# Optimization experiments

Measured on AMD Instinct MI355X. Metric: run time of the kernel, lower is better.

The kernel has to match this reference:

```python
import jax, jax.numpy as jnp
import numpy as np

B, S, H = 1, 2048, 4096
NQ, NKV = 32, 8
HD = H // NQ  # 128


def _rope_tables(seq_len, head_dim, base=10000.0):
    inv_freq = 1.0 / (base ** (np.arange(0, head_dim, 2, dtype=np.float32) / head_dim))
    t = np.arange(seq_len, dtype=np.float32)
    freqs = np.outer(t, inv_freq)  # (S, HD/2)
    emb = np.concatenate([freqs, freqs], axis=-1)  # (S, HD)
    return jnp.asarray(np.cos(emb)), jnp.asarray(np.sin(emb))


def setup_inputs() -> dict:
    key = jax.random.key(0)
    ks = jax.random.split(key, 5)
    cos, sin = _rope_tables(S, HD)
    scale = 1.0 / np.sqrt(H)
    return {
        "hidden_states": jax.random.normal(ks[0], (B, S, H), dtype=jnp.float32),
        "cos": cos,
        "sin": sin,
        "wq": jax.random.normal(ks[1], (H, NQ * HD), dtype=jnp.float32) * scale,
        "wk": jax.random.normal(ks[2], (H, NKV * HD), dtype=jnp.float32) * scale,
        "wv": jax.random.normal(ks[3], (H, NKV * HD), dtype=jnp.float32) * scale,
        "wo": jax.random.normal(ks[4], (NQ * HD, H), dtype=jnp.float32) * scale,
    }


def _rotate_half(x):
    x1, x2 = jnp.split(x, 2, axis=-1)
    return jnp.concatenate([-x2, x1], axis=-1)


def reference(hidden_states, cos, sin, wq, wk, wv, wo):
    b, s, _ = hidden_states.shape
    q = (hidden_states @ wq).reshape(b, s, NQ, HD)
    k = (hidden_states @ wk).reshape(b, s, NKV, HD)
    v = (hidden_states @ wv).reshape(b, s, NKV, HD)
    c = cos[None, :, None, :]
    sn = sin[None, :, None, :]
    q = q * c + _rotate_half(q) * sn
    k = k * c + _rotate_half(k) * sn
    groups = NQ // NKV
    # GQA: compute scores per kv-head group without materially repeating K/V beyond einsum
    q = q.reshape(b, s, NKV, groups, HD)
    # scores: (b, kv_head, group, s_q, s_k)
    scores = jnp.einsum("bqhgd,bkhd->bhgqk", q, k) / jnp.sqrt(jnp.asarray(HD, q.dtype))
    causal = jnp.tril(jnp.ones((s, s), dtype=bool))
    scores = jnp.where(causal[None, None, None], scores, jnp.finfo(scores.dtype).min)
    attn = jax.nn.softmax(scores, axis=-1)
    out = jnp.einsum("bhgqk,bkhd->bqhgd", attn, v)  # (b, s, kv_h, g, d)
    out = out.reshape(b, s, NQ * HD)
    return out @ wo
```

## Files before the change

kernel.cpp:

```cpp
#include <hip/hip_runtime.h>
#include <hip/hip_bf16.h>
#include <math.h>

#define S_LEN 2048
#define HDIM  4096
#define NQ_H  32
#define NKV_H 8
#define HD_   128
#define DQ (NQ_H*HD_)
#define DKV (NKV_H*HD_)
#define NFUSE (DQ + 2*DKV)

typedef unsigned short u16;
typedef unsigned int   u32;
typedef __attribute__((ext_vector_type(8))) short short8;
typedef __attribute__((ext_vector_type(4))) float f32x4;

__device__ __forceinline__ u16 bf16_rne(float x) {
    u32 u = __float_as_uint(x);
    u = (u + 0x7FFFu + ((u >> 16) & 1u)) >> 16;
    return (u16)u;
}
__device__ __forceinline__ float bf16_to_f(u16 h) {
    return __uint_as_float(((u32)h) << 16);
}
__device__ __forceinline__ void glds16(const u16* g, u16* l) {
    __builtin_amdgcn_global_load_lds(
        (const __attribute__((address_space(1))) u32*)g,
        (__attribute__((address_space(3))) u32*)l,
        16, 0, 0);
}

__global__ __launch_bounds__(256) void cvt_bf16(const float* __restrict__ in,
                                                u16* __restrict__ out, int n) {
    int i = (blockIdx.x * 256 + threadIdx.x) * 8;
    if (i >= n) return;
    float4 a = *(const float4*)&in[i];
    float4 b = *(const float4*)&in[i + 4];
    u16 h[8];
    h[0] = bf16_rne(a.x); h[1] = bf16_rne(a.y); h[2] = bf16_rne(a.z); h[3] = bf16_rne(a.w);
    h[4] = bf16_rne(b.x); h[5] = bf16_rne(b.y); h[6] = bf16_rne(b.z); h[7] = bf16_rne(b.w);
    *(uint4*)&out[i] = *(uint4*)h;
}

__global__ __launch_bounds__(256) void add_f32(const float* __restrict__ p1,
                                               float* __restrict__ out, int n) {
    int i = (blockIdx.x * 256 + threadIdx.x) * 4;
    if (i >= n) return;
    float4 a = *(const float4*)&out[i];
    float4 b = *(const float4*)&p1[i];
    a.x += b.x; a.y += b.y; a.z += b.z; a.w += b.w;
    *(float4*)&out[i] = a;
}

__global__ __launch_bounds__(256) void cvtT_qkv(const float* __restrict__ wq,
                                                const float* __restrict__ wk,
                                                const float* __restrict__ wv,
                                                u16* __restrict__ WT) {
    __shared__ float tile[32][33];
    const int n0g = blockIdx.x * 32;
    const int k0  = blockIdx.y * 32;
    const float* W; int Nsrc, nloc0;
    if (n0g < DQ)            { W = wq; Nsrc = DQ;  nloc0 = n0g; }
    else if (n0g < DQ + DKV) { W = wk; Nsrc = DKV; nloc0 = n0g - DQ; }
    else                     { W = wv; Nsrc = DKV; nloc0 = n0g - DQ - DKV; }
    const int tx = threadIdx.x & 31;
    const int ty = threadIdx.x >> 5;
#pragma unroll
    for (int i = 0; i < 4; ++i)
        tile[ty + 8 * i][tx] = W[(size_t)(k0 + ty + 8 * i) * Nsrc + nloc0 + tx];
    __syncthreads();
#pragma unroll
    for (int i = 0; i < 4; ++i) {
        int r = ty + 8 * i;
        WT[(size_t)(n0g + r) * HDIM + k0 + tx] = bf16_rne(tile[tx][r]);
    }
}

#define AOFFU(par, mh) ((par) * 16384 + (mh) * 8192)
#define BOFFU(par, nh) (32768 + (par) * 16384 + (nh) * 8192)

__global__ __launch_bounds__(512, 2) void gemm_qkv256(const u16* __restrict__ A,
                                                      const u16* __restrict__ BT,
                                                      u16* __restrict__ qb,
                                                      u16* __restrict__ kb,
                                                      u16* __restrict__ vb,
                                                      const float* __restrict__ wo,
                                                      u16* __restrict__ woT) {
    const int K  = HDIM;
    const int NT = K / 64;
    __shared__ u16 smem[65536] __attribute__((aligned(16)));

    const int id = blockIdx.x;
    const int t  = threadIdx.x;

    if (id >= 192) {
        const int b  = id - 192;
        const int n0 = b * 64;
        float* tile = (float*)smem;
        const int r  = t >> 3;
        const int c8 = (t & 7) * 8;
        for (int k0 = 0; k0 < DQ; k0 += 64) {
            float4 x0 = *(const float4*)&wo[(size_t)(k0 + r) * HDIM + n0 + c8];
            float4 x1 = *(const float4*)&wo[(size_t)(k0 + r) * HDIM + n0 + c8 + 4];
            float* tr = &tile[r * 68 + c8];
            tr[0] = x0.x; tr[1] = x0.y; tr[2] = x0.z; tr[3] = x0.w;
            tr[4] = x1.x; tr[5] = x1.y; tr[6] = x1.z; tr[7] = x1.w;
            __syncthreads();
            u16 h[8];
#pragma unroll
            for (int j = 0; j < 8; ++j) h[j] = bf16_rne(tile[(c8 + j) * 68 + r]);
            *(uint4*)&woT[(size_t)(n0 + r) * DQ + k0 + c8] = *(uint4*)h;
            __syncthreads();
        }
        return;
    }

    const int w    = t >> 6;
    const int lane = t & 63;
    const int wm   = w >> 2;
    const int wn   = w & 3;
    const int fr   = lane & 15;
    const int quad = lane >> 4;
    const int m0   = (id / 24) * 256;
    const int n0   = (id % 24) * 256;

    const int lrow = lane >> 3;
    const int lc   = (lane & 7) ^ lrow;
    const u16* const baseA = A  + (size_t)(m0 + w * 16 + lrow) * K + lc * 8;
    const u16* const baseB = BT + (size_t)(n0 + w * 16 + lrow) * K + lc * 8;
    const int wdst = w * 1024;

    const int pc0  = (quad ^ (fr & 7)) * 8;
    const int pc1  = pc0 ^ 32;
    const int aRow = (wm * 64 + fr) * 64;
    const int bRow = (wn * 32 + fr) * 64;

    f32x4 acc[2][2][4][2];
#pragma unroll
    for (int a = 0; a < 2; ++a)
#pragma unroll
        for (int b = 0; b < 2; ++b)
#pragma unroll
            for (int c = 0; c < 4; ++c)
#pragma unroll
                for (int d = 0; d < 2; ++d) acc[a][b][c][d] = (f32x4)0.f;

    short8 ar0[4][2], ar1[4][2], br[2][2];

    auto stA = [&](int off, int tile, int mh) {
        const u16* g = baseA + (size_t)mh * 128 * K + tile * 64;
        glds16(g,                 smem + off + wdst);
        glds16(g + (size_t)8 * K, smem + off + wdst + 512);
    };
    auto stB = [&](int off, int tile, int nh) {
        const u16* g = baseB + (size_t)nh * 128 * K + tile * 64;
        glds16(g,                 smem + off + wdst);
        glds16(g + (size_t)8 * K, smem + off + wdst + 512);
    };
    auto rdA = [&](short8 (&d)[4][2], int off) {
#pragma unroll
        for (int mr = 0; mr < 4; ++mr) {
            d[mr][0] = *(const short8*)&smem[off + aRow + mr * 1024 + pc0];
            d[mr][1] = *(const short8*)&smem[off + aRow + mr * 1024 + pc1];
        }
    };
    auto rdB = [&](short8 (&d)[2][2], int off) {
#pragma unroll
        for (int nc = 0; nc < 2; ++nc) {
            d[nc][0] = *(const short8*)&smem[off + bRow + nc * 1024 + pc0];
            d[nc][1] = *(const short8*)&smem[off + bRow + nc * 1024 + pc1];
        }
    };
    auto mma = [&](short8 (&a)[4][2], short8 (&b)[2][2], f32x4 (&c)[4][2]) {
        __builtin_amdgcn_s_setprio(1);
#pragma unroll
        for (int mr = 0; mr < 4; ++mr)
#pragma unroll
            for (int nc = 0; nc < 2; ++nc) {
                c[mr][nc] = __builtin_amdgcn_mfma_f32_16x16x32_bf16(a[mr][0], b[nc][0], c[mr][nc], 0, 0, 0);
                c[mr][nc] = __builtin_amdgcn_mfma_f32_16x16x32_bf16(a[mr][1], b[nc][1], c[mr][nc], 0, 0, 0);
            }
        __builtin_amdgcn_s_setprio(0);
    };

    stA(AOFFU(0,0), 0, 0);
    stB(BOFFU(0,0), 0, 0);
    stA(AOFFU(0,1), 0, 1);
    stB(BOFFU(0,1), 0, 1);
    stA(AOFFU(1,0), 1, 0);
    stB(BOFFU(1,0), 1, 0);
    stA(AOFFU(1,1), 1, 1);
    asm volatile("s_waitcnt vmcnt(6)" ::: "memory");
    __builtin_amdgcn_s_barrier();

    for (int T = 0; T < NT; T += 2) {
        const int ts2 = (T + 2 < NT) ? T + 2 : NT - 1;
        const int ts3 = (T + 3 < NT) ? T + 3 : NT - 1;
        rdA(ar0, AOFFU(0,0));
        rdB(br,  BOFFU(0,0));
        stB(BOFFU(1,1), T + 1, 1);
        __builtin_amdgcn_s_barrier();
        asm volatile("s_waitcnt lgkmcnt(0)" ::: "memory");
        mma(ar0, br, acc[0][0]);
        __builtin_amdgcn_s_barrier();
        rdA(ar1, AOFFU(0,1));
        stA(AOFFU(0,0), ts2, 0);
        __builtin_amdgcn_s_barrier();
        asm volatile("s_waitcnt lgkmcnt(0)" ::: "memory");
        mma(ar1, br, acc[1][0]);
        __builtin_amdgcn_s_barrier();
        rdB(br, BOFFU(0,1));
        stB(BOFFU(0,0), ts2, 0);
        __builtin_amdgcn_s_barrier();
        asm volatile("s_waitcnt lgkmcnt(0)" ::: "memory");
        mma(ar1, br, acc[1][1]);
        __builtin_amdgcn_s_barrier();
        stA(AOFFU(0,1), ts2, 1);
        __builtin_amdgcn_s_barrier();
        asm volatile("s_waitcnt lgkmcnt(0)" ::: "memory");
        mma(ar0, br, acc[0][1]);
        asm volatile("s_waitcnt vmcnt(6)" ::: "memory");
        __builtin_amdgcn_s_barrier();
        rdA(ar0, AOFFU(1,0));
        rdB(br,  BOFFU(1,0));
        stB(BOFFU(0,1), ts2, 1);
        __builtin_amdgcn_s_barrier();
        asm volatile("s_waitcnt lgkmcnt(0)" ::: "memory");
        mma(ar0, br, acc[0][0]);
        __builtin_amdgcn_s_barrier();
        rdA(ar1, AOFFU(1,1));
        stA(AOFFU(1,0), ts3, 0);
        __builtin_amdgcn_s_barrier();
        asm volatile("s_waitcnt lgkmcnt(0)" ::: "memory");
        mma(ar1, br, acc[1][0]);
        __builtin_amdgcn_s_barrier();
        rdB(br, BOFFU(1,1));
        stB(BOFFU(1,0), ts3, 0);
        __builtin_amdgcn_s_barrier();
        asm volatile("s_waitcnt lgkmcnt(0)" ::: "memory");
        mma(ar1, br, acc[1][1]);
        __builtin_amdgcn_s_barrier();
        stA(AOFFU(1,1), ts3, 1);
        __builtin_amdgcn_s_barrier();
        asm volatile("s_waitcnt lgkmcnt(0)" ::: "memory");
        mma(ar0, br, acc[0][1]);
        asm volatile("s_waitcnt vmcnt(6)" ::: "memory");
        __builtin_amdgcn_s_barrier();
    }

    u16* dst; int stride, nbase;
    if (n0 < DQ)            { dst = qb; stride = DQ;  nbase = n0; }
    else if (n0 < DQ + DKV) { dst = kb; stride = DKV; nbase = n0 - DQ; }
    else                    { dst = vb; stride = DKV; nbase = n0 - DQ - DKV; }

    const int col = lane & 15;
    const int rq  = (lane >> 4) * 4;
#pragma unroll
    for (int mh = 0; mh < 2; ++mh)
#pragma unroll
        for (int nh = 0; nh < 2; ++nh)
#pragma unroll
            for (int mr = 0; mr < 4; ++mr)
#pragma unroll
                for (int nc = 0; nc < 2; ++nc)
#pragma unroll
                    for (int i = 0; i < 4; ++i)
                        dst[(size_t)(m0 + mh * 128 + wm * 64 + mr * 16 + rq + i) * stride
                            + nbase + nh * 128 + wn * 32 + nc * 16 + col] =
                            bf16_rne(acc[mh][nh][mr][nc][i]);
}

__global__ __launch_bounds__(512, 2) void gemm_out256(const u16* __restrict__ A,
                                                      const u16* __restrict__ BT,
                                                      float* __restrict__ C,
                                                      float* __restrict__ P1) {
    const int LDA = DQ;
    const int NT  = 32;
    __shared__ u16 smem[65536] __attribute__((aligned(16)));

    const int t    = threadIdx.x;
    const int w    = t >> 6;
    const int lane = t & 63;
    const int wm   = w >> 2;
    const int wn   = w & 3;
    const int fr   = lane & 15;
    const int quad = lane >> 4;
    const int m0   = blockIdx.y * 256;
    const int n0   = blockIdx.x * 256;
    const int kz   = blockIdx.z * 2048;

    const int lrow = lane >> 3;
    const int lc   = (lane & 7) ^ lrow;
    const u16* const baseA = A  + (size_t)(m0 + w * 16 + lrow) * LDA + kz + lc * 8;
    const u16* const baseB = BT + (size_t)(n0 + w * 16 + lrow) * LDA + kz + lc * 8;
    const int wdst = w * 1024;

    const int pc0  = (quad ^ (fr & 7)) * 8;
    const int pc1  = pc0 ^ 32;
    const int aRow = (wm * 64 + fr) * 64;
    const int bRow = (wn * 32 + fr) * 64;

    f32x4 acc[2][2][4][2];
#pragma unroll
    for (int a = 0; a < 2; ++a)
#pragma unroll
        for (int b = 0; b < 2; ++b)
#pragma unroll
            for (int c = 0; c < 4; ++c)
#pragma unroll
                for (int d = 0; d < 2; ++d) acc[a][b][c][d] = (f32x4)0.f;

    short8 ar0[4][2], ar1[4][2], br[2][2];

    auto stA = [&](int off, int tile, int mh) {
        const u16* g = baseA + (size_t)mh * 128 * LDA + tile * 64;
        glds16(g,                   smem + off + wdst);
        glds16(g + (size_t)8 * LDA, smem + off + wdst + 512);
    };
    auto stB = [&](int off, int tile, int nh) {
        const u16* g = baseB + (size_t)nh * 128 * LDA + tile * 64;
        glds16(g,                   smem + off + wdst);
        glds16(g + (size_t)8 * LDA, smem + off + wdst + 512);
    };
    auto rdA = [&](short8 (&d)[4][2], int off) {
#pragma unroll
        for (int mr = 0; mr < 4; ++mr) {
            d[mr][0] = *(const short8*)&smem[off + aRow + mr * 1024 + pc0];
            d[mr][1] = *(const short8*)&smem[off + aRow + mr * 1024 + pc1];
        }
    };
    auto rdB = [&](short8 (&d)[2][2], int off) {
#pragma unroll
        for (int nc = 0; nc < 2; ++nc) {
            d[nc][0] = *(const short8*)&smem[off + bRow + nc * 1024 + pc0];
            d[nc][1] = *(const short8*)&smem[off + bRow + nc * 1024 + pc1];
        }
    };
    auto mma = [&](short8 (&a)[4][2], short8 (&b)[2][2], f32x4 (&c)[4][2]) {
        __builtin_amdgcn_s_setprio(1);
#pragma unroll
        for (int mr = 0; mr < 4; ++mr)
#pragma unroll
            for (int nc = 0; nc < 2; ++nc) {
                c[mr][nc] = __builtin_amdgcn_mfma_f32_16x16x32_bf16(a[mr][0], b[nc][0], c[mr][nc], 0, 0, 0);
                c[mr][nc] = __builtin_amdgcn_mfma_f32_16x16x32_bf16(a[mr][1], b[nc][1], c[mr][nc], 0, 0, 0);
            }
        __builtin_amdgcn_s_setprio(0);
    };

    stA(AOFFU(0,0), 0, 0);
    stB(BOFFU(0,0), 0, 0);
    stA(AOFFU(0,1), 0, 1);
    stB(BOFFU(0,1), 0, 1);
    stA(AOFFU(1,0), 1, 0);
    stB(BOFFU(1,0), 1, 0);
    stA(AOFFU(1,1), 1, 1);
    asm volatile("s_waitcnt vmcnt(6)" ::: "memory");
    __builtin_amdgcn_s_barrier();

    for (int T = 0; T < NT; T += 2) {
        const int ts2 = (T + 2 < NT) ? T + 2 : NT - 1;
        const int ts3 = (T + 3 < NT) ? T + 3 : NT - 1;
        rdA(ar0, AOFFU(0,0));
        rdB(br,  BOFFU(0,0));
        stB(BOFFU(1,1), T + 1, 1);
        __builtin_amdgcn_s_barrier();
        asm volatile("s_waitcnt lgkmcnt(0)" ::: "memory");
        mma(ar0, br, acc[0][0]);
        __builtin_amdgcn_s_barrier();
        rdA(ar1, AOFFU(0,1));
        stA(AOFFU(0,0), ts2, 0);
        __builtin_amdgcn_s_barrier();
        asm volatile("s_waitcnt lgkmcnt(0)" ::: "memory");
        mma(ar1, br, acc[1][0]);
        __builtin_amdgcn_s_barrier();
        rdB(br, BOFFU(0,1));
        stB(BOFFU(0,0), ts2, 0);
        __builtin_amdgcn_s_barrier();
        asm volatile("s_waitcnt lgkmcnt(0)" ::: "memory");
        mma(ar1, br, acc[1][1]);
        __builtin_amdgcn_s_barrier();
        stA(AOFFU(0,1), ts2, 1);
        __builtin_amdgcn_s_barrier();
        asm volatile("s_waitcnt lgkmcnt(0)" ::: "memory");
        mma(ar0, br, acc[0][1]);
        asm volatile("s_waitcnt vmcnt(6)" ::: "memory");
        __builtin_amdgcn_s_barrier();
        rdA(ar0, AOFFU(1,0));
        rdB(br,  BOFFU(1,0));
        stB(BOFFU(0,1), ts2, 1);
        __builtin_amdgcn_s_barrier();
        asm volatile("s_waitcnt lgkmcnt(0)" ::: "memory");
        mma(ar0, br, acc[0][0]);
        __builtin_amdgcn_s_barrier();
        rdA(ar1, AOFFU(1,1));
        stA(AOFFU(1,0), ts3, 0);
        __builtin_amdgcn_s_barrier();
        asm volatile("s_waitcnt lgkmcnt(0)" ::: "memory");
        mma(ar1, br, acc[1][0]);
        __builtin_amdgcn_s_barrier();
        rdB(br, BOFFU(1,1));
        stB(BOFFU(1,0), ts3, 0);
        __builtin_amdgcn_s_barrier();
        asm volatile("s_waitcnt lgkmcnt(0)" ::: "memory");
        mma(ar1, br, acc[1][1]);
        __builtin_amdgcn_s_barrier();
        stA(AOFFU(1,1), ts3, 1);
        __builtin_amdgcn_s_barrier();
        asm volatile("s_waitcnt lgkmcnt(0)" ::: "memory");
        mma(ar0, br, acc[0][1]);
        asm volatile("s_waitcnt vmcnt(6)" ::: "memory");
        __builtin_amdgcn_s_barrier();
    }

    float* const dst = (blockIdx.z == 0) ? C : P1;
    const int col = lane & 15;
    const int rq  = (lane >> 4) * 4;
#pragma unroll
    for (int mh = 0; mh < 2; ++mh)
#pragma unroll
        for (int nh = 0; nh < 2; ++nh)
#pragma unroll
            for (int mr = 0; mr < 4; ++mr)
#pragma unroll
                for (int nc = 0; nc < 2; ++nc)
#pragma unroll
                    for (int i = 0; i < 4; ++i)
                        dst[(size_t)(m0 + mh * 128 + wm * 64 + mr * 16 + rq + i) * HDIM
                            + n0 + nh * 128 + wn * 32 + nc * 16 + col] =
                            acc[mh][nh][mr][nc][i];
}

__global__ __launch_bounds__(256) void rope2(u16* __restrict__ q, u16* __restrict__ k,
                                             const float* __restrict__ cosT,
                                             const float* __restrict__ sinT) {
    int idx = blockIdx.x * 256 + threadIdx.x;
    int d4   = (idx & 15) * 4;
    int rest = idx >> 4;
    int head = rest % (NQ_H + NKV_H);
    int s    = rest / (NQ_H + NKV_H);
    u16* base = (head < NQ_H)
        ? q + ((size_t)s * NQ_H + head) * HD_
        : k + ((size_t)s * NKV_H + (head - NQ_H)) * HD_;
    float4 c  = *(const float4*)&cosT[s * HD_ + d4];
    float4 sn = *(const float4*)&sinT[s * HD_ + d4];
    u16 lo[4], hi[4];
    *(uint2*)lo = *(uint2*)&base[d4];
    *(uint2*)hi = *(uint2*)&base[d4 + 64];
    float cs[4] = {c.x, c.y, c.z, c.w};
    float ss[4] = {sn.x, sn.y, sn.z, sn.w};
    u16 nlo[4], nhi[4];
#pragma unroll
    for (int j = 0; j < 4; ++j) {
        float x1 = bf16_to_f(lo[j]);
        float x2 = bf16_to_f(hi[j]);
        nlo[j] = bf16_rne(x1 * cs[j] - x2 * ss[j]);
        nhi[j] = bf16_rne(x2 * cs[j] + x1 * ss[j]);
    }
    *(uint2*)&base[d4]      = *(uint2*)nlo;
    *(uint2*)&base[d4 + 64] = *(uint2*)nhi;
}

__global__ __launch_bounds__(256) void transpose_v(const u16* __restrict__ V,
                                                   u16* __restrict__ Vt) {
    __shared__ u16 tile[64][72];
    const int s0  = blockIdx.x * 64;
    const int kvh = blockIdx.y >> 1;
    const int d0  = (blockIdx.y & 1) * 64;
    const int t = threadIdx.x;
    const int chunk = t & 7;
    const int row   = t >> 3;
#pragma unroll
    for (int p = 0; p < 2; ++p) {
        int s = row + 32 * p;
        uint4 x = *(const uint4*)&V[(size_t)(s0 + s) * DKV + kvh * HD_ + d0 + chunk * 8];
        *(uint4*)&tile[s][chunk * 8] = x;
    }
    __syncthreads();
#pragma unroll
    for (int p = 0; p < 2; ++p) {
        int d = row + 32 * p;
        u16 tmp[8];
#pragma unroll
        for (int j = 0; j < 8; ++j) tmp[j] = tile[chunk * 8 + j][d];
        *(uint4*)&Vt[(size_t)(kvh * HD_ + d0 + d) * S_LEN + s0 + chunk * 8] = *(uint4*)tmp;
    }
}

#define QSTR 136
#define PSTR 76
__global__ __launch_bounds__(512, 4) void attn_mfma(const u16* __restrict__ Q,
                                                    const u16* __restrict__ K,
                                                    const u16* __restrict__ Vt,
                                                    u16* __restrict__ O) {
    __shared__ u16 smem[26112] __attribute__((aligned(16)));
    u16* sK  = smem;
    u16* sVt = smem + 8192;
    u16* sP  = smem + 16384;
    u16* sQ  = sVt;

    const int id  = blockIdx.x;
    const int h   = id & 31;
    const int qt  = (id < 256) ? (15 - (id >> 5)) : ((id - 256) >> 5);
    const int kvh = h >> 2;
    const int q0  = qt * 128;
    const int t    = threadIdx.x;
    const int w    = t >> 6;
    const int lane = t & 63;
    const int fr   = lane & 15;
    const int quad = lane >> 4;
    const int nkt  = 2 * qt + 2;

    const float K1 = 0.12751744154f;
    const float K2 = 11.5415603267f;

    const int kRow  = t >> 3;
    const int kC    = t & 7;
    const int kLds0 = kRow * 128 + (((2 * kC + 0) ^ (kRow & 7)) * 8);
    const int kLds1 = kRow * 128 + (((2 * kC + 1) ^ (kRow & 7)) * 8);
    const u16* const kGp = K + (size_t)kRow * DKV + (size_t)kvh * HD_ + kC * 16;

    const int vRow  = t >> 2;
    const int vC    = t & 3;
    const int vLds0 = vRow * 64 + (((2 * vC + 0) ^ (vRow & 7)) * 8);
    const int vLds1 = vRow * 64 + (((2 * vC + 1) ^ (vRow & 7)) * 8);
    const u16* const vGp = Vt + ((size_t)kvh * HD_ + vRow) * S_LEN + vC * 16;

    uint4 kr0 = *(const uint4*)(kGp);
    uint4 kr1 = *(const uint4*)(kGp + 8);
    uint4 vr0 = *(const uint4*)(vGp);
    uint4 vr1 = *(const uint4*)(vGp + 8);

    {
        const int col  = t & 15;
        const int row4 = t >> 4;
#pragma unroll
        for (int p = 0; p < 4; ++p) {
            int row = row4 + 32 * p;
            uint4 xv = *(const uint4*)&Q[(size_t)(q0 + row) * DQ + h * HD_ + col * 8];
            *(uint4*)&sQ[row * QSTR + col * 8] = xv;
        }
    }
    __syncthreads();

    short8 aq[4];
#pragma unroll
    for (int ks = 0; ks < 4; ++ks)
        aq[ks] = *(const short8*)&sQ[(16 * w + fr) * QSTR + ks * 32 + quad * 8];

    float lrow[4] = {0.f, 0.f, 0.f, 0.f};
    f32x4 oacc[8];
#pragma unroll
    for (int n8 = 0; n8 < 8; ++n8) oacc[n8] = (f32x4)0.f;

    u16* const sPw   = sP + w * (16 * PSTR);
    const int  qwTop = q0 + 16 * w;

    for (int kt = 0; kt < nkt; ++kt) {
        const int k0 = kt * 64;
        __syncthreads();

        *(uint4*)&sK[kLds0]  = kr0;
        *(uint4*)&sK[kLds1]  = kr1;
        *(uint4*)&sVt[vLds0] = vr0;
        *(uint4*)&sVt[vLds1] = vr1;
        if (kt + 1 < nkt) {
            const u16* kp = kGp + (size_t)(k0 + 64) * DKV;
            kr0 = *(const uint4*)(kp);
            kr1 = *(const uint4*)(kp + 8);
            const u16* vp = vGp + (k0 + 64);
            vr0 = *(const uint4*)(vp);
            vr1 = *(const uint4*)(vp + 8);
        }
        __syncthreads();

        if (k0 <= qwTop + 15) {
            f32x4 sacc[4];
#pragma unroll
            for (int nt = 0; nt < 4; ++nt) sacc[nt] = (f32x4)0.f;
            __builtin_amdgcn_s_setprio(1);
#pragma unroll
            for (int ks = 0; ks < 4; ++ks)
#pragma unroll
                for (int nt = 0; nt < 4; ++nt) {
                    const short8 bk = *(const short8*)
                        &sK[(nt * 16 + fr) * 128 + (((ks * 4 + quad) ^ (fr & 7)) * 8)];
                    sacc[nt] = __builtin_amdgcn_mfma_f32_16x16x32_bf16(aq[ks], bk, sacc[nt], 0, 0, 0);
                }
            __builtin_amdgcn_s_setprio(0);

            if (k0 + 63 > qwTop) {
#pragma unroll
                for (int nt = 0; nt < 4; ++nt) {
                    int key = k0 + nt * 16 + fr;
#pragma unroll
                    for (int i = 0; i < 4; ++i)
                        if (key > qwTop + quad * 4 + i) sacc[nt][i] = -INFINITY;
                }
            }

#pragma unroll
            for (int nt = 0; nt < 4; ++nt)
#pragma unroll
                for (int i = 0; i < 4; ++i) {
                    float p = __builtin_amdgcn_exp2f(fmaf(sacc[nt][i], K1, -K2));
                    lrow[i] += p;
                    sPw[(quad * 4 + i) * PSTR + nt * 16 + fr] = bf16_rne(p);
                }

            __builtin_amdgcn_s_setprio(1);
#pragma unroll
            for (int ks2 = 0; ks2 < 2; ++ks2) {
                const short8 ap = *(const short8*)&sPw[fr * PSTR + ks2 * 32 + quad * 8];
#pragma unroll
                for (int n8 = 0; n8 < 8; ++n8) {
                    const short8 bv = *(const short8*)
                        &sVt[(n8 * 16 + fr) * 64 + (((ks2 * 4 + quad) ^ (fr & 7)) * 8)];
                    oacc[n8] = __builtin_amdgcn_mfma_f32_16x16x32_bf16(ap, bv, oacc[n8], 0, 0, 0);
                }
            }
            __builtin_amdgcn_s_setprio(0);
        }
    }

#pragma unroll
    for (int i = 0; i < 4; ++i) {
        lrow[i] += __shfl_xor(lrow[i], 1);
        lrow[i] += __shfl_xor(lrow[i], 2);
        lrow[i] += __shfl_xor(lrow[i], 4);
        lrow[i] += __shfl_xor(lrow[i], 8);
    }
#pragma unroll
    for (int i = 0; i < 4; ++i) {
        float inv = 1.f / lrow[i];
        size_t base = (size_t)(qwTop + quad * 4 + i) * DQ + h * HD_;
#pragma unroll
        for (int n8 = 0; n8 < 8; ++n8)
            O[base + n8 * 16 + fr] = bf16_rne(oacc[n8][i] * inv);
    }
}

extern "C" void kernel_launch(void* const* d_in, const int* in_sizes, int n_in,
                              void* d_out, int out_size, void* d_ws, size_t ws_size,
                              hipStream_t stream) {
    const float* X    = (const float*)d_in[0];
    const float* cosT = (const float*)d_in[1];
    const float* sinT = (const float*)d_in[2];
    const float* wq   = (const float*)d_in[3];
    const float* wk   = (const float*)d_in[4];
    const float* wv   = (const float*)d_in[5];
    const float* wo   = (const float*)d_in[6];
    float* out = (float*)d_out;

    const size_t SDQ  = (size_t)S_LEN * DQ;
    const size_t SDKV = (size_t)S_LEN * DKV;
    const size_t WQKV = (size_t)HDIM * NFUSE;

    u16* Xb  = (u16*)d_ws;
    u16* qb  = Xb + SDQ;
    u16* kb  = qb + SDQ;
    u16* vb  = kb + SDKV;
    u16* vtb = vb + SDKV;
    u16* aob = vtb + SDKV;
    u16* WT  = aob + SDQ;
    u16* woT = WT + WQKV;

    float* P1 = (float*)d_ws;

    dim3 blk(256);

    cvt_bf16<<<SDQ / 2048, blk, 0, stream>>>(X, Xb, (int)SDQ);
    cvtT_qkv<<<dim3(NFUSE / 32, HDIM / 32), blk, 0, stream>>>(wq, wk, wv, WT);

    gemm_qkv256<<<dim3(256), dim3(512), 0, stream>>>(Xb, WT, qb, kb, vb, wo, woT);

    rope2<<<(S_LEN * (NQ_H + NKV_H) * 16) / 256, blk, 0, stream>>>(qb, kb, cosT, sinT);

    transpose_v<<<dim3(S_LEN / 64, NKV_H * 2), blk, 0, stream>>>(vb, vtb);

    attn_mfma<<<dim3(512), dim3(512), 0, stream>>>(qb, kb, vtb, aob);

    gemm_out256<<<dim3(HDIM / 256, S_LEN / 256, 2), dim3(512), 0, stream>>>(aob, woT, out, P1);
    add_f32<<<(S_LEN * HDIM) / 1024, blk, 0, stream>>>(P1, out, S_LEN * HDIM);
}
```

Measured before the change: 462.0 us.

## Fuse prep kernels and reduce split-K output in place via flag sync

The X-to-bf16 conversion and the QKV weight transpose-convert are merged into one launch, and so are RoPE and the V transpose. The split-K output GEMM no longer writes a partial buffer for a separate add kernel. Instead each second-half block spins on a per-tile flag that its first-half partner sets after storing, then adds its accumulators into the output in place. The wo transpose tile padding also changes from 68 to 65 to reduce LDS bank conflicts. Together these remove three launches and a full fp32 read/write pass. In exchange the output GEMM relies on inter-block spin waits, which assume the z=0 blocks are scheduled first, and it needs a memset of the flags.

```diff
diff --git a/kernel.cpp b/kernel.cpp
--- a/kernel.cpp
+++ b/kernel.cpp
@@ -31,35 +31,27 @@
         16, 0, 0);
 }
 
-__global__ __launch_bounds__(256) void cvt_bf16(const float* __restrict__ in,
-                                                u16* __restrict__ out, int n) {
-    int i = (blockIdx.x * 256 + threadIdx.x) * 8;
-    if (i >= n) return;
-    float4 a = *(const float4*)&in[i];
-    float4 b = *(const float4*)&in[i + 4];
-    u16 h[8];
-    h[0] = bf16_rne(a.x); h[1] = bf16_rne(a.y); h[2] = bf16_rne(a.z); h[3] = bf16_rne(a.w);
-    h[4] = bf16_rne(b.x); h[5] = bf16_rne(b.y); h[6] = bf16_rne(b.z); h[7] = bf16_rne(b.w);
-    *(uint4*)&out[i] = *(uint4*)h;
-}
-
-__global__ __launch_bounds__(256) void add_f32(const float* __restrict__ p1,
-                                               float* __restrict__ out, int n) {
-    int i = (blockIdx.x * 256 + threadIdx.x) * 4;
-    if (i >= n) return;
-    float4 a = *(const float4*)&out[i];
-    float4 b = *(const float4*)&p1[i];
-    a.x += b.x; a.y += b.y; a.z += b.z; a.w += b.w;
-    *(float4*)&out[i] = a;
-}
-
-__global__ __launch_bounds__(256) void cvtT_qkv(const float* __restrict__ wq,
-                                                const float* __restrict__ wk,
-                                                const float* __restrict__ wv,
-                                                u16* __restrict__ WT) {
+__global__ __launch_bounds__(256) void cvt_all(const float* __restrict__ X,
+                                               u16* __restrict__ Xb,
+                                               const float* __restrict__ wq,
+                                               const float* __restrict__ wk,
+                                               const float* __restrict__ wv,
+                                               u16* __restrict__ WT) {
     __shared__ float tile[32][33];
-    const int n0g = blockIdx.x * 32;
-    const int k0  = blockIdx.y * 32;
+    const int bid = blockIdx.x;
+    if (bid < 4096) {
+        int i = (bid * 256 + threadIdx.x) * 8;
+        float4 a = *(const float4*)&X[i];
+        float4 b = *(const float4*)&X[i + 4];
+        u16 h[8];
+        h[0] = bf16_rne(a.x); h[1] = bf16_rne(a.y); h[2] = bf16_rne(a.z); h[3] = bf16_rne(a.w);
+        h[4] = bf16_rne(b.x); h[5] = bf16_rne(b.y); h[6] = bf16_rne(b.z); h[7] = bf16_rne(b.w);
+        *(uint4*)&Xb[i] = *(uint4*)h;
+        return;
+    }
+    const int wid = bid - 4096;
+    const int n0g = (wid % 192) * 32;
+    const int k0  = (wid / 192) * 32;
     const float* W; int Nsrc, nloc0;
     if (n0g < DQ)            { W = wq; Nsrc = DQ;  nloc0 = n0g; }
     else if (n0g < DQ + DKV) { W = wk; Nsrc = DKV; nloc0 = n0g - DQ; }
@@ -103,13 +95,13 @@
         for (int k0 = 0; k0 < DQ; k0 += 64) {
             float4 x0 = *(const float4*)&wo[(size_t)(k0 + r) * HDIM + n0 + c8];
             float4 x1 = *(const float4*)&wo[(size_t)(k0 + r) * HDIM + n0 + c8 + 4];
-            float* tr = &tile[r * 68 + c8];
+            float* tr = &tile[r * 65 + c8];
             tr[0] = x0.x; tr[1] = x0.y; tr[2] = x0.z; tr[3] = x0.w;
             tr[4] = x1.x; tr[5] = x1.y; tr[6] = x1.z; tr[7] = x1.w;
             __syncthreads();
             u16 h[8];
 #pragma unroll
-            for (int j = 0; j < 8; ++j) h[j] = bf16_rne(tile[(c8 + j) * 68 + r]);
+            for (int j = 0; j < 8; ++j) h[j] = bf16_rne(tile[(c8 + j) * 65 + r]);
             *(uint4*)&woT[(size_t)(n0 + r) * DQ + k0 + c8] = *(uint4*)h;
             __syncthreads();
         }
@@ -274,7 +266,7 @@
 __global__ __launch_bounds__(512, 2) void gemm_out256(const u16* __restrict__ A,
                                                       const u16* __restrict__ BT,
                                                       float* __restrict__ C,
-                                                      float* __restrict__ P1) {
+                                                      u32* __restrict__ flags) {
     const int LDA = DQ;
     const int NT  = 32;
     __shared__ u16 smem[65536] __attribute__((aligned(16)));
@@ -289,6 +281,7 @@
     const int m0   = blockIdx.y * 256;
     const int n0   = blockIdx.x * 256;
     const int kz   = blockIdx.z * 2048;
+    const int tile_id = blockIdx.y * 16 + blockIdx.x;
 
     const int lrow = lane >> 3;
     const int lc   = (lane & 7) ^ lrow;
@@ -414,61 +407,89 @@
         __builtin_amdgcn_s_barrier();
     }
 
-    float* const dst = (blockIdx.z == 0) ? C : P1;
     const int col = lane & 15;
     const int rq  = (lane >> 4) * 4;
-#pragma unroll
-    for (int mh = 0; mh < 2; ++mh)
-#pragma unroll
-        for (int nh = 0; nh < 2; ++nh)
-#pragma unroll
-            for (int mr = 0; mr < 4; ++mr)
-#pragma unroll
-                for (int nc = 0; nc < 2; ++nc)
-#pragma unroll
-                    for (int i = 0; i < 4; ++i)
-                        dst[(size_t)(m0 + mh * 128 + wm * 64 + mr * 16 + rq + i) * HDIM
-                            + n0 + nh * 128 + wn * 32 + nc * 16 + col] =
-                            acc[mh][nh][mr][nc][i];
-}
-
-__global__ __launch_bounds__(256) void rope2(u16* __restrict__ q, u16* __restrict__ k,
-                                             const float* __restrict__ cosT,
-                                             const float* __restrict__ sinT) {
-    int idx = blockIdx.x * 256 + threadIdx.x;
-    int d4   = (idx & 15) * 4;
-    int rest = idx >> 4;
-    int head = rest % (NQ_H + NKV_H);
-    int s    = rest / (NQ_H + NKV_H);
-    u16* base = (head < NQ_H)
-        ? q + ((size_t)s * NQ_H + head) * HD_
-        : k + ((size_t)s * NKV_H + (head - NQ_H)) * HD_;
-    float4 c  = *(const float4*)&cosT[s * HD_ + d4];
-    float4 sn = *(const float4*)&sinT[s * HD_ + d4];
-    u16 lo[4], hi[4];
-    *(uint2*)lo = *(uint2*)&base[d4];
-    *(uint2*)hi = *(uint2*)&base[d4 + 64];
-    float cs[4] = {c.x, c.y, c.z, c.w};
-    float ss[4] = {sn.x, sn.y, sn.z, sn.w};
-    u16 nlo[4], nhi[4];
-#pragma unroll
-    for (int j = 0; j < 4; ++j) {
-        float x1 = bf16_to_f(lo[j]);
-        float x2 = bf16_to_f(hi[j]);
-        nlo[j] = bf16_rne(x1 * cs[j] - x2 * ss[j]);
-        nhi[j] = bf16_rne(x2 * cs[j] + x1 * ss[j]);
-    }
-    *(uint2*)&base[d4]      = *(uint2*)nlo;
-    *(uint2*)&base[d4 + 64] = *(uint2*)nhi;
-}
-
-__global__ __launch_bounds__(256) void transpose_v(const u16* __restrict__ V,
-                                                   u16* __restrict__ Vt) {
+    if (blockIdx.z == 0) {
+#pragma unroll
+        for (int mh = 0; mh < 2; ++mh)
+#pragma unroll
+            for (int nh = 0; nh < 2; ++nh)
+#pragma unroll
+                for (int mr = 0; mr < 4; ++mr)
+#pragma unroll
+                    for (int nc = 0; nc < 2; ++nc)
+#pragma unroll
+                        for (int i = 0; i < 4; ++i)
+                            C[(size_t)(m0 + mh * 128 + wm * 64 + mr * 16 + rq + i) * HDIM
+                              + n0 + nh * 128 + wn * 32 + nc * 16 + col] =
+                                acc[mh][nh][mr][nc][i];
+        __syncthreads();
+        if (t == 0)
+            __hip_atomic_store(&flags[tile_id], 1u, __ATOMIC_RELEASE, __HIP_MEMORY_SCOPE_AGENT);
+    } else {
+        if (t == 0) {
+            while (__hip_atomic_load(&flags[tile_id], __ATOMIC_ACQUIRE, __HIP_MEMORY_SCOPE_AGENT) == 0u)
+                __builtin_amdgcn_s_sleep(2);
+        }
+        __syncthreads();
+#pragma unroll
+        for (int mh = 0; mh < 2; ++mh)
+#pragma unroll
+            for (int nh = 0; nh < 2; ++nh)
+#pragma unroll
+                for (int mr = 0; mr < 4; ++mr)
+#pragma unroll
+                    for (int nc = 0; nc < 2; ++nc)
+#pragma unroll
+                        for (int i = 0; i < 4; ++i) {
+                            size_t off = (size_t)(m0 + mh * 128 + wm * 64 + mr * 16 + rq + i) * HDIM
+                                         + n0 + nh * 128 + wn * 32 + nc * 16 + col;
+                            C[off] += acc[mh][nh][mr][nc][i];
+                        }
+    }
+}
+
+__global__ __launch_bounds__(256) void rope_tv(u16* __restrict__ q, u16* __restrict__ k,
+                                               const float* __restrict__ cosT,
+                                               const float* __restrict__ sinT,
+                                               const u16* __restrict__ V,
+                                               u16* __restrict__ Vt) {
     __shared__ u16 tile[64][72];
-    const int s0  = blockIdx.x * 64;
-    const int kvh = blockIdx.y >> 1;
-    const int d0  = (blockIdx.y & 1) * 64;
+    const int bid = blockIdx.x;
     const int t = threadIdx.x;
+    if (bid < 5120) {
+        int idx = bid * 256 + t;
+        int d4   = (idx & 15) * 4;
+        int rest = idx >> 4;
+        int head = rest % (NQ_H + NKV_H);
+        int s    = rest / (NQ_H + NKV_H);
+        u16* base = (head < NQ_H)
+            ? q + ((size_t)s * NQ_H + head) * HD_
+            : k + ((size_t)s * NKV_H + (head - NQ_H)) * HD_;
+        float4 c  = *(const float4*)&cosT[s * HD_ + d4];
+        float4 sn = *(const float4*)&sinT[s * HD_ + d4];
+        u16 lo[4], hi[4];
+        *(uint2*)lo = *(uint2*)&base[d4];
+        *(uint2*)hi = *(uint2*)&base[d4 + 64];
+        float cs[4] = {c.x, c.y, c.z, c.w};
+        float ss[4] = {sn.x, sn.y, sn.z, sn.w};
+        u16 nlo[4], nhi[4];
+#pragma unroll
+        for (int j = 0; j < 4; ++j) {
+            float x1 = bf16_to_f(lo[j]);
+            float x2 = bf16_to_f(hi[j]);
+            nlo[j] = bf16_rne(x1 * cs[j] - x2 * ss[j]);
+            nhi[j] = bf16_rne(x2 * cs[j] + x1 * ss[j]);
+        }
+        *(uint2*)&base[d4]      = *(uint2*)nlo;
+        *(uint2*)&base[d4 + 64] = *(uint2*)nhi;
+        return;
+    }
+    const int b   = bid - 5120;
+    const int s0  = (b & 31) * 64;
+    const int yy  = b >> 5;
+    const int kvh = yy >> 1;
+    const int d0  = (yy & 1) * 64;
     const int chunk = t & 7;
     const int row   = t >> 3;
 #pragma unroll
@@ -666,21 +687,18 @@
     u16* WT  = aob + SDQ;
     u16* woT = WT + WQKV;
 
-    float* P1 = (float*)d_ws;
+    u32* flags = (u32*)d_ws;
 
     dim3 blk(256);
 
-    cvt_bf16<<<SDQ / 2048, blk, 0, stream>>>(X, Xb, (int)SDQ);
-    cvtT_qkv<<<dim3(NFUSE / 32, HDIM / 32), blk, 0, stream>>>(wq, wk, wv, WT);
+    cvt_all<<<dim3(4096 + 24576), blk, 0, stream>>>(X, Xb, wq, wk, wv, WT);
 
     gemm_qkv256<<<dim3(256), dim3(512), 0, stream>>>(Xb, WT, qb, kb, vb, wo, woT);
 
-    rope2<<<(S_LEN * (NQ_H + NKV_H) * 16) / 256, blk, 0, stream>>>(qb, kb, cosT, sinT);
-
-    transpose_v<<<dim3(S_LEN / 64, NKV_H * 2), blk, 0, stream>>>(vb, vtb);
+    rope_tv<<<dim3(5120 + 512), blk, 0, stream>>>(qb, kb, cosT, sinT, vb, vtb);
 
     attn_mfma<<<dim3(512), dim3(512), 0, stream>>>(qb, kb, vtb, aob);
 
-    gemm_out256<<<dim3(HDIM / 256, S_LEN / 256, 2), dim3(512), 0, stream>>>(aob, woT, out, P1);
-    add_f32<<<(S_LEN * HDIM) / 1024, blk, 0, stream>>>(P1, out, S_LEN * HDIM);
-}
+    hipMemsetAsync(flags, 0, 128 * sizeof(u32), stream);
+    gemm_out256<<<dim3(HDIM / 256, S_LEN / 256, 2), dim3(512), 0, stream>>>(aob, woT, out, flags);
+}
```

Result: slower. 480.7 us (+4.0%).
